# Kernel tuning notes

Hardware: AMD Instinct MI355X
Metric: run time of the kernel (lower is better)

Reference implementation:

```python
import jax, jax.numpy as jnp
import numpy as np

EMBED_DIM = 1024
NUM_HEADS = 16
HEAD_DIM = EMBED_DIM // NUM_HEADS
N, S = 4, 2048


def setup_inputs() -> dict:
    key = jax.random.key(0)
    ks = jax.random.split(key, 11)
    s = 1.0 / np.sqrt(EMBED_DIM)
    inp = {
        'query': jax.random.normal(ks[0], (N, S, EMBED_DIM), jnp.float32),
        'key': jax.random.normal(ks[1], (N, S, EMBED_DIM), jnp.float32),
        'value': jax.random.normal(ks[2], (N, S, EMBED_DIM), jnp.float32),
        'wq': jax.random.normal(ks[3], (EMBED_DIM, EMBED_DIM), jnp.float32) * s,
        'bq': jnp.zeros((EMBED_DIM,), jnp.float32),
        'wk': jax.random.normal(ks[4], (EMBED_DIM, EMBED_DIM), jnp.float32) * s,
        'bk': jnp.zeros((EMBED_DIM,), jnp.float32),
        'wv': jax.random.normal(ks[5], (EMBED_DIM, EMBED_DIM), jnp.float32) * s,
        'bv': jnp.zeros((EMBED_DIM,), jnp.float32),
        'wo': jax.random.normal(ks[6], (EMBED_DIM, EMBED_DIM), jnp.float32) * s,
        'bo': jnp.zeros((EMBED_DIM,), jnp.float32),
    }
    return inp


def reference(query, key, value, wq, bq, wk, bk, wv, bv, wo, bo):
    n = query.shape[0]
    # projections: y = x @ W^T + b (torch nn.Linear convention)
    Q = query @ wq.T + bq
    K = key @ wk.T + bk
    V = value @ wv.T + bv
    # [n, h, s, d]
    Q = Q.reshape(n, -1, NUM_HEADS, HEAD_DIM).transpose(0, 2, 1, 3)
    K = K.reshape(n, -1, NUM_HEADS, HEAD_DIM).transpose(0, 2, 1, 3)
    V = V.reshape(n, -1, NUM_HEADS, HEAD_DIM).transpose(0, 2, 1, 3)
    energy = jnp.einsum('nhqd,nhkd->nhqk', Q, K)
    attn = jax.nn.softmax(energy / jnp.sqrt(jnp.float32(HEAD_DIM)), axis=-1)
    out = jnp.einsum('nhqk,nhkd->nhqd', attn, V)
    out = out.transpose(0, 2, 1, 3).reshape(n, -1, NUM_HEADS * HEAD_DIM)
    return out @ wo.T + bo
```

## Files before the change

### kernel.cpp

```cpp
#include <hip/hip_runtime.h>
#include <hip/hip_bf16.h>

#define EMBED 1024
#define SEQ   2048
#define NB    4
#define NH    16
#define HD    64
#define MROWS (NB*SEQ)
#define WELEM (EMBED*EMBED)

typedef __attribute__((ext_vector_type(4))) float  f32x4;
typedef __attribute__((ext_vector_type(8))) short  s16x8;

#define MFMA16(a,b,c) __builtin_amdgcn_mfma_f32_16x16x32_bf16((a),(b),(c),0,0,0)

__device__ __forceinline__ unsigned short f2bf(float f) {
    union { float f; unsigned int u; } v; v.f = f;
    unsigned int r = v.u + 0x7fffu + ((v.u >> 16) & 1u);
    return (unsigned short)(r >> 16);
}
__device__ __forceinline__ unsigned int cvtpk(float a, float b) {
    unsigned int r;
    asm("v_cvt_pk_bf16_f32 %0, %1, %2" : "=v"(r) : "v"(a), "v"(b));
    return r;
}
__device__ __forceinline__ float exp2r(float x) {
    float r;
    asm("v_exp_f32 %0, %1" : "=v"(r) : "v"(x));
    return r;
}
__device__ __forceinline__ void gload16(const void* g, void* l) {
    __builtin_amdgcn_global_load_lds(
        (const __attribute__((address_space(1))) void*)g,
        (__attribute__((address_space(3))) void*)l, 16, 0, 0);
}

#define SC2 0.18033688f

__global__ __launch_bounds__(256) void conv_w(
    const float* __restrict__ wq, const float* __restrict__ wk,
    const float* __restrict__ wv, const float* __restrict__ wo,
    unsigned short* __restrict__ Wbf)
{
    const int i   = blockIdx.x*256 + threadIdx.x;
    const int seg = i >> 17;
    const int off = i & 131071;
    const float* src = seg == 0 ? wq : (seg == 1 ? wk : (seg == 2 ? wv : wo));
    const float sc   = seg == 0 ? SC2 : 1.f;
    const float4 a = *(const float4*)(src + (size_t)off*8);
    const float4 b = *(const float4*)(src + (size_t)off*8 + 4);
    uint4 o;
    o.x = cvtpk(a.x*sc, a.y*sc); o.y = cvtpk(a.z*sc, a.w*sc);
    o.z = cvtpk(b.x*sc, b.y*sc); o.w = cvtpk(b.z*sc, b.w*sc);
    *(uint4*)(Wbf + (size_t)seg*WELEM + (size_t)off*8) = o;
}

template<int WMODE>
__global__ __launch_bounds__(256) void qkv_fused(
    const float* __restrict__ Aq, const float* __restrict__ Ak,
    const float* __restrict__ Av,
    const float* __restrict__ wq, const float* __restrict__ wk,
    const float* __restrict__ wv, const unsigned short* __restrict__ Wbf,
    const float* __restrict__ bq, const float* __restrict__ bk,
    const float* __restrict__ bv,
    unsigned short* __restrict__ Qp, unsigned short* __restrict__ Kp,
    unsigned short* __restrict__ Vt)
{
    __shared__ unsigned short Ald[128*72];
    __shared__ unsigned short Bld[WMODE ? 128*64 : 128*72];
    const int t   = threadIdx.x;
    const int bm  = blockIdx.x, bn = blockIdx.y;
    const int sel = bn >> 3, bnl = bn & 7;
    const float* Af   = sel == 0 ? Aq : (sel == 1 ? Ak : Av);
    const float* Wf   = sel == 0 ? wq : (sel == 1 ? wk : wv);
    const unsigned short* Wb = Wbf + (size_t)sel*WELEM;
    const float* bias = sel == 0 ? bq : (sel == 1 ? bk : bv);

    const int wid = t >> 6, lane = t & 63, l15 = lane & 15, blk = lane >> 4;
    const int wr  = wid >> 1, wc = wid & 1;

    f32x4 acc[4][4] = {};

    for (int kt = 0; kt < EMBED/64; ++kt) {
        if (WMODE == 1) {
            #pragma unroll
            for (int i = 0; i < 4; ++i) {
                const int u = i*256 + t, row = u >> 3, slot = u & 7;
                const unsigned short* src = Wb + (size_t)(bnl*128+row)*EMBED
                                               + kt*64 + (slot ^ (row & 7))*8;
                gload16(src, (char*)Bld + i*4096 + wid*1024);
            }
        }
        #pragma unroll
        for (int i = 0; i < 8; ++i) {
            int f = t + 256*i, row = f >> 4, c4 = f & 15;
            float4 v = *(const float4*)(Af + (size_t)(bm*128+row)*EMBED + kt*64 + c4*4);
            *(uint2*)&Ald[row*72 + c4*4] = make_uint2(cvtpk(v.x,v.y), cvtpk(v.z,v.w));
        }
        if (WMODE == 0) {
            #pragma unroll
            for (int i = 0; i < 8; ++i) {
                int f = t + 256*i, row = f >> 4, c4 = f & 15;
                float4 v = *(const float4*)(Wf + (size_t)(bnl*128+row)*EMBED + kt*64 + c4*4);
                *(uint2*)&Bld[row*72 + c4*4] = make_uint2(cvtpk(v.x,v.y), cvtpk(v.z,v.w));
            }
        } else {
            asm volatile("s_waitcnt vmcnt(0)" ::: "memory");
        }
        __syncthreads();
        #pragma unroll
        for (int ks = 0; ks < 2; ++ks) {
            s16x8 af[4], bf[4];
            #pragma unroll
            for (int mt = 0; mt < 4; ++mt)
                af[mt] = *(const s16x8*)&Ald[(wr*64 + mt*16 + l15)*72 + ks*32 + blk*8];
            #pragma unroll
            for (int nt = 0; nt < 4; ++nt) {
                const int rb = wc*64 + nt*16 + l15;
                if (WMODE == 1)
                    bf[nt] = *(const s16x8*)((const char*)Bld + rb*128
                                 + ((ks*64 + blk*16) ^ ((rb & 7) << 4)));
                else
                    bf[nt] = *(const s16x8*)&Bld[rb*72 + ks*32 + blk*8];
            }
            #pragma unroll
            for (int mt = 0; mt < 4; ++mt)
                #pragma unroll
                for (int nt = 0; nt < 4; ++nt)
                    acc[mt][nt] = MFMA16(af[mt], bf[nt], acc[mt][nt]);
        }
        __syncthreads();
    }

    const float scale = (sel == 0) ? SC2 : 1.0f;
    float bv4[4];
    #pragma unroll
    for (int nt = 0; nt < 4; ++nt) {
        float bb = bias[bnl*128 + wc*64 + nt*16 + l15];
        bv4[nt] = (WMODE == 1) ? bb*scale : bb;
    }

    #pragma unroll
    for (int mt = 0; mt < 4; ++mt) {
        #pragma unroll
        for (int nt = 0; nt < 4; ++nt) {
            const int m0 = bm*128 + wr*64 + mt*16 + blk*4;
            const int n  = bnl*128 + wc*64 + nt*16 + l15;
            f32x4 a = acc[mt][nt];
            if (sel < 2) {
                unsigned short* Yb = (sel == 0) ? Qp : Kp;
                #pragma unroll
                for (int r = 0; r < 4; ++r) {
                    float val = (WMODE == 1) ? (a[r] + bv4[nt])
                                             : (a[r] + bv4[nt]) * scale;
                    Yb[(size_t)(m0+r)*EMBED + n] = f2bf(val);
                }
            } else {
                const int b = m0 >> 11, s = m0 & (SEQ-1);
                const int h = n >> 6,  d = n & (HD-1);
                ushort4 pk;
                pk.x = f2bf(a[0] + bv4[nt]); pk.y = f2bf(a[1] + bv4[nt]);
                pk.z = f2bf(a[2] + bv4[nt]); pk.w = f2bf(a[3] + bv4[nt]);
                *(ushort4*)&Vt[(((size_t)b*NH + h)*HD + d)*SEQ + s] = pk;
            }
        }
    }
}

template<int WMODE>
__global__ __launch_bounds__(256) void gemm_out(
    const unsigned short* __restrict__ Ab, const float* __restrict__ W,
    const unsigned short* __restrict__ Wb,
    const float* __restrict__ bias, float* __restrict__ Yf)
{
    __shared__ unsigned short Ald[128*64];
    __shared__ unsigned short Bld[WMODE ? 128*64 : 128*72];
    const int t   = threadIdx.x;
    const int bm  = blockIdx.x, bn = blockIdx.y;
    const int wid = t >> 6, lane = t & 63, l15 = lane & 15, blk = lane >> 4;
    const int wr  = wid >> 1, wc = wid & 1;

    f32x4 acc[4][4] = {};

    for (int kt = 0; kt < EMBED/64; ++kt) {
        #pragma unroll
        for (int i = 0; i < 4; ++i) {
            const int u = i*256 + t, row = u >> 3, slot = u & 7;
            const unsigned short* src = Ab + (size_t)(bm*128+row)*EMBED
                                           + kt*64 + (slot ^ (row & 7))*8;
            gload16(src, (char*)Ald + i*4096 + wid*1024);
        }
        if (WMODE == 1) {
            #pragma unroll
            for (int i = 0; i < 4; ++i) {
                const int u = i*256 + t, row = u >> 3, slot = u & 7;
                const unsigned short* src = Wb + (size_t)(bn*128+row)*EMBED
                                               + kt*64 + (slot ^ (row & 7))*8;
                gload16(src, (char*)Bld + i*4096 + wid*1024);
            }
        } else {
            #pragma unroll
            for (int i = 0; i < 8; ++i) {
                int f = t + 256*i, row = f >> 4, c4 = f & 15;
                float4 v = *(const float4*)(W + (size_t)(bn*128+row)*EMBED + kt*64 + c4*4);
                *(uint2*)&Bld[row*72 + c4*4] = make_uint2(cvtpk(v.x,v.y), cvtpk(v.z,v.w));
            }
        }
        asm volatile("s_waitcnt vmcnt(0)" ::: "memory");
        __syncthreads();
        #pragma unroll
        for (int ks = 0; ks < 2; ++ks) {
            s16x8 af[4], bf[4];
            #pragma unroll
            for (int mt = 0; mt < 4; ++mt) {
                const int ra = wr*64 + mt*16 + l15;
                af[mt] = *(const s16x8*)((const char*)Ald + ra*128
                             + ((ks*64 + blk*16) ^ ((ra & 7) << 4)));
            }
            #pragma unroll
            for (int nt = 0; nt < 4; ++nt) {
                const int rb = wc*64 + nt*16 + l15;
                if (WMODE == 1)
                    bf[nt] = *(const s16x8*)((const char*)Bld + rb*128
                                 + ((ks*64 + blk*16) ^ ((rb & 7) << 4)));
                else
                    bf[nt] = *(const s16x8*)&Bld[rb*72 + ks*32 + blk*8];
            }
            #pragma unroll
            for (int mt = 0; mt < 4; ++mt)
                #pragma unroll
                for (int nt = 0; nt < 4; ++nt)
                    acc[mt][nt] = MFMA16(af[mt], bf[nt], acc[mt][nt]);
        }
        __syncthreads();
    }

    float bv4[4];
    #pragma unroll
    for (int nt = 0; nt < 4; ++nt)
        bv4[nt] = bias[bn*128 + wc*64 + nt*16 + l15];

    #pragma unroll
    for (int mt = 0; mt < 4; ++mt)
        #pragma unroll
        for (int nt = 0; nt < 4; ++nt) {
            const int m0 = bm*128 + wr*64 + mt*16 + blk*4;
            const int n  = bn*128 + wc*64 + nt*16 + l15;
            f32x4 a = acc[mt][nt];
            #pragma unroll
            for (int r = 0; r < 4; ++r)
                Yf[(size_t)(m0+r)*EMBED + n] = a[r] + bv4[nt];
        }
}

__global__ __launch_bounds__(512) void attn_fwd(
    const unsigned short* __restrict__ Qp,
    const unsigned short* __restrict__ Kp,
    const unsigned short* __restrict__ Vt,
    unsigned short* __restrict__ ctx)
{
    __shared__ unsigned short Kld[2][64*64];
    __shared__ unsigned short Vld[2][64*64];
    __shared__ unsigned short Pld[8][32*64];

    const int t = threadIdx.x, wid = t >> 6, lane = t & 63;
    const int l15 = lane & 15, blk = lane >> 4;
    const int bh = blockIdx.x, qb = blockIdx.y;
    const int b = bh >> 4, h = bh & (NH-1);
    const int q0 = qb*256 + wid*32;

    s16x8 qf[2][2];
    #pragma unroll
    for (int qs = 0; qs < 2; ++qs) {
        const unsigned short* qp = Qp + (size_t)(b*SEQ + q0 + qs*16 + l15)*EMBED + h*HD;
        qf[qs][0] = *(const s16x8*)(qp + blk*8);
        qf[qs][1] = *(const s16x8*)(qp + 32 + blk*8);
    }

    const unsigned short* kb = Kp + (size_t)b*SEQ*EMBED + h*HD;
    const unsigned short* vb = Vt + (size_t)bh*HD*SEQ;

    const int u  = wid*64 + lane;
    const int r0 = u >> 3;
    const int s0 = ((((u&7)<<4) ^ ((r0&7)<<4)) >> 1);
    const unsigned short* kS = kb + (size_t)r0*EMBED + s0;
    const unsigned short* vS = vb + (size_t)r0*SEQ  + s0;

    unsigned short* pl = &Pld[wid][0];
    const int rc0 = (blk*16) ^ ((l15 & 7) << 4);
    const int rc1 = rc0 ^ 64;

    s16x8 onesf;
    #pragma unroll
    for (int i = 0; i < 8; ++i) onesf[i] = (short)0x3F80;

    f32x4 o[2][4] = {};
    f32x4 sacc[2] = {};

    gload16(kS, (char*)Kld[0] + wid*1024);
    gload16(vS, (char*)Vld[0] + wid*1024);
    asm volatile("s_waitcnt vmcnt(0)" ::: "memory");
    __syncthreads();

    int cur = 0;
    for (int tt = 0; tt < SEQ/64; ++tt) {
        if (tt + 1 < SEQ/64) {
            const size_t ko = (size_t)(tt+1)*64;
            gload16(kS + ko*EMBED, (char*)Kld[cur^1] + wid*1024);
            gload16(vS + ko,       (char*)Vld[cur^1] + wid*1024);
        }

        const char* kbase = (const char*)Kld[cur];
        const char* vbase = (const char*)Vld[cur];

        f32x4 sc[2][4];
        #pragma unroll
        for (int qs = 0; qs < 2; ++qs)
            #pragma unroll
            for (int kt = 0; kt < 4; ++kt)
                sc[qs][kt] = f32x4{0.f,0.f,0.f,0.f};
        __builtin_amdgcn_s_setprio(1);
        #pragma unroll
        for (int kt = 0; kt < 4; ++kt) {
            const char* krow = kbase + (kt*16 + l15)*128;
            s16x8 ka0 = *(const s16x8*)(krow + rc0);
            s16x8 ka1 = *(const s16x8*)(krow + rc1);
            #pragma unroll
            for (int qs = 0; qs < 2; ++qs) {
                sc[qs][kt] = MFMA16(ka0, qf[qs][0], sc[qs][kt]);
                sc[qs][kt] = MFMA16(ka1, qf[qs][1], sc[qs][kt]);
            }
        }
        __builtin_amdgcn_s_setprio(0);

        #pragma unroll
        for (int qs = 0; qs < 2; ++qs) {
            #pragma unroll
            for (int kt = 0; kt < 4; ++kt) {
                const float e0 = exp2r(sc[qs][kt][0]);
                const float e1 = exp2r(sc[qs][kt][1]);
                const float e2 = exp2r(sc[qs][kt][2]);
                const float e3 = exp2r(sc[qs][kt][3]);
                const int off = (qs*16 + l15)*128 + ((kt*32 + blk*8) ^ ((l15 & 7) << 4));
                *(uint2*)((char*)pl + off) = make_uint2(cvtpk(e0,e1), cvtpk(e2,e3));
            }
        }

        s16x8 pa[2][2];
        #pragma unroll
        for (int qs = 0; qs < 2; ++qs) {
            const char* prow = (const char*)pl + (qs*16 + l15)*128;
            pa[qs][0] = *(const s16x8*)(prow + rc0);
            pa[qs][1] = *(const s16x8*)(prow + rc1);
        }
        __builtin_amdgcn_s_setprio(1);
        #pragma unroll
        for (int qs = 0; qs < 2; ++qs) {
            sacc[qs] = MFMA16(pa[qs][0], onesf, sacc[qs]);
            sacc[qs] = MFMA16(pa[qs][1], onesf, sacc[qs]);
        }
        #pragma unroll
        for (int dt = 0; dt < 4; ++dt) {
            const char* vrow = vbase + (dt*16 + l15)*128;
            s16x8 vb0 = *(const s16x8*)(vrow + rc0);
            s16x8 vb1 = *(const s16x8*)(vrow + rc1);
            #pragma unroll
            for (int qs = 0; qs < 2; ++qs) {
                o[qs][dt] = MFMA16(pa[qs][0], vb0, o[qs][dt]);
                o[qs][dt] = MFMA16(pa[qs][1], vb1, o[qs][dt]);
            }
        }
        __builtin_amdgcn_s_setprio(0);

        asm volatile("s_waitcnt vmcnt(0)" ::: "memory");
        __syncthreads();
        cur ^= 1;
    }

    #pragma unroll
    for (int qs = 0; qs < 2; ++qs) {
        float li[4];
        #pragma unroll
        for (int r = 0; r < 4; ++r) li[r] = 1.f / sacc[qs][r];
        unsigned short* cp = ctx + (size_t)(b*SEQ + q0 + qs*16)*EMBED + h*HD;
        #pragma unroll
        for (int dt = 0; dt < 4; ++dt)
            #pragma unroll
            for (int r = 0; r < 4; ++r)
                cp[(size_t)(blk*4 + r)*EMBED + dt*16 + l15] = f2bf(o[qs][dt][r] * li[r]);
    }
}

extern "C" void kernel_launch(void* const* d_in, const int* in_sizes, int n_in,
                              void* d_out, int out_size, void* d_ws, size_t ws_size,
                              hipStream_t stream)
{
    const float* q  = (const float*)d_in[0];
    const float* k  = (const float*)d_in[1];
    const float* v  = (const float*)d_in[2];
    const float* wq = (const float*)d_in[3];
    const float* bq = (const float*)d_in[4];
    const float* wk = (const float*)d_in[5];
    const float* bk = (const float*)d_in[6];
    const float* wv = (const float*)d_in[7];
    const float* bv = (const float*)d_in[8];
    const float* wo = (const float*)d_in[9];
    const float* bo = (const float*)d_in[10];

    unsigned short* Qp  = (unsigned short*)d_out;
    unsigned short* Kp  = Qp + (size_t)MROWS*EMBED;
    unsigned short* Vt  = (unsigned short*)d_ws;
    unsigned short* ctx = Vt + (size_t)MROWS*EMBED;
    unsigned short* Wbf = ctx + (size_t)MROWS*EMBED;
    float* out = (float*)d_out;

    const bool pre = ws_size >= (size_t)40*1024*1024;

    dim3 tpb(256);
    if (pre) {
        conv_w<<<2048, tpb, 0, stream>>>(wq, wk, wv, wo, Wbf);
        qkv_fused<1><<<dim3(MROWS/128, 24), tpb, 0, stream>>>(
            q, k, v, wq, wk, wv, Wbf, bq, bk, bv, Qp, Kp, Vt);
    } else {
        qkv_fused<0><<<dim3(MROWS/128, 24), tpb, 0, stream>>>(
            q, k, v, wq, wk, wv, Wbf, bq, bk, bv, Qp, Kp, Vt);
    }
    attn_fwd<<<dim3(NB*NH, SEQ/256), dim3(512), 0, stream>>>(Qp, Kp, Vt, ctx);
    if (pre) {
        gemm_out<1><<<dim3(MROWS/128, EMBED/128), tpb, 0, stream>>>(
            ctx, wo, Wbf + (size_t)3*WELEM, bo, out);
    } else {
        gemm_out<0><<<dim3(MROWS/128, EMBED/128), tpb, 0, stream>>>(
            ctx, wo, Wbf, bo, out);
    }
}
```

Before: 182.3 us.

## Keep softmax probabilities in registers using K=16 MFMA for PV

```diff
diff --git a/kernel.cpp b/kernel.cpp
--- a/kernel.cpp
+++ b/kernel.cpp
@@ -11,8 +11,24 @@
 
 typedef __attribute__((ext_vector_type(4))) float  f32x4;
 typedef __attribute__((ext_vector_type(8))) short  s16x8;
+typedef __attribute__((ext_vector_type(4))) short  s16x4;
+typedef __attribute__((ext_vector_type(2))) unsigned int u32x2;
 
 #define MFMA16(a,b,c) __builtin_amdgcn_mfma_f32_16x16x32_bf16((a),(b),(c),0,0,0)
+
+#if __has_builtin(__builtin_amdgcn_mfma_f32_16x16x16bf16_1k)
+#define MFMAK16(a,b,c) __builtin_amdgcn_mfma_f32_16x16x16bf16_1k((a),(b),(c),0,0,0)
+#elif __has_builtin(__builtin_amdgcn_mfma_f32_16x16x16_bf16)
+#define MFMAK16(a,b,c) __builtin_amdgcn_mfma_f32_16x16x16_bf16((a),(b),(c),0,0,0)
+#else
+static __device__ __forceinline__ f32x4 mfmak16_asm(s16x4 a, s16x4 b, f32x4 c) {
+    f32x4 d;
+    asm volatile("v_mfma_f32_16x16x16_bf16 %0, %1, %2, %3\n\ts_nop 7\n\ts_nop 7"
+                 : "=v"(d) : "v"(a), "v"(b), "v"(c));
+    return d;
+}
+#define MFMAK16(a,b,c) mfmak16_asm((a),(b),(c))
+#endif
 
 __device__ __forceinline__ unsigned short f2bf(float f) {
     union { float f; unsigned int u; } v; v.f = f;
@@ -261,7 +277,6 @@
 {
     __shared__ unsigned short Kld[2][64*64];
     __shared__ unsigned short Vld[2][64*64];
-    __shared__ unsigned short Pld[8][32*64];
 
     const int t = threadIdx.x, wid = t >> 6, lane = t & 63;
     const int l15 = lane & 15, blk = lane >> 4;
@@ -286,13 +301,12 @@
     const unsigned short* kS = kb + (size_t)r0*EMBED + s0;
     const unsigned short* vS = vb + (size_t)r0*SEQ  + s0;
 
-    unsigned short* pl = &Pld[wid][0];
     const int rc0 = (blk*16) ^ ((l15 & 7) << 4);
     const int rc1 = rc0 ^ 64;
 
-    s16x8 onesf;
-    #pragma unroll
-    for (int i = 0; i < 8; ++i) onesf[i] = (short)0x3F80;
+    s16x4 ones4;
+    #pragma unroll
+    for (int i = 0; i < 4; ++i) ones4[i] = (short)0x3F80;
 
     f32x4 o[2][4] = {};
     f32x4 sacc[2] = {};
@@ -333,41 +347,33 @@
         }
         __builtin_amdgcn_s_setprio(0);
 
-        #pragma unroll
-        for (int qs = 0; qs < 2; ++qs) {
+        s16x4 pa[2][4];
+        #pragma unroll
+        for (int qs = 0; qs < 2; ++qs)
             #pragma unroll
             for (int kt = 0; kt < 4; ++kt) {
-                const float e0 = exp2r(sc[qs][kt][0]);
-                const float e1 = exp2r(sc[qs][kt][1]);
-                const float e2 = exp2r(sc[qs][kt][2]);
-                const float e3 = exp2r(sc[qs][kt][3]);
-                const int off = (qs*16 + l15)*128 + ((kt*32 + blk*8) ^ ((l15 & 7) << 4));
-                *(uint2*)((char*)pl + off) = make_uint2(cvtpk(e0,e1), cvtpk(e2,e3));
-            }
-        }
-
-        s16x8 pa[2][2];
-        #pragma unroll
-        for (int qs = 0; qs < 2; ++qs) {
-            const char* prow = (const char*)pl + (qs*16 + l15)*128;
-            pa[qs][0] = *(const s16x8*)(prow + rc0);
-            pa[qs][1] = *(const s16x8*)(prow + rc1);
-        }
+                union { u32x2 u; s16x4 s; } c;
+                c.u[0] = cvtpk(exp2r(sc[qs][kt][0]), exp2r(sc[qs][kt][1]));
+                c.u[1] = cvtpk(exp2r(sc[qs][kt][2]), exp2r(sc[qs][kt][3]));
+                pa[qs][kt] = c.s;
+            }
+
         __builtin_amdgcn_s_setprio(1);
         #pragma unroll
-        for (int qs = 0; qs < 2; ++qs) {
-            sacc[qs] = MFMA16(pa[qs][0], onesf, sacc[qs]);
-            sacc[qs] = MFMA16(pa[qs][1], onesf, sacc[qs]);
-        }
+        for (int qs = 0; qs < 2; ++qs)
+            #pragma unroll
+            for (int kt = 0; kt < 4; ++kt)
+                sacc[qs] = MFMAK16(pa[qs][kt], ones4, sacc[qs]);
         #pragma unroll
         for (int dt = 0; dt < 4; ++dt) {
             const char* vrow = vbase + (dt*16 + l15)*128;
-            s16x8 vb0 = *(const s16x8*)(vrow + rc0);
-            s16x8 vb1 = *(const s16x8*)(vrow + rc1);
-            #pragma unroll
-            for (int qs = 0; qs < 2; ++qs) {
-                o[qs][dt] = MFMA16(pa[qs][0], vb0, o[qs][dt]);
-                o[qs][dt] = MFMA16(pa[qs][1], vb1, o[qs][dt]);
+            #pragma unroll
+            for (int kt = 0; kt < 4; ++kt) {
+                s16x4 vb4 = *(const s16x4*)(vrow
+                               + ((kt*32 + blk*8) ^ ((l15 & 7) << 4)));
+                #pragma unroll
+                for (int qs = 0; qs < 2; ++qs)
+                    o[qs][dt] = MFMAK16(pa[qs][kt], vb4, o[qs][dt]);
             }
         }
         __builtin_amdgcn_s_setprio(0);
```

New measurement: 189.1 us. 1.04x slower.
